# Kernel optimization log

Hardware: AMD Instinct MI355X
Metric: run time of the kernel (lower is better)

Reference implementation:

```python
import jax, jax.numpy as jnp
import numpy as np

B, S, D = 4, 2048, 1024
H, HD = 16, 64  # num_head, head_dim


def setup_inputs() -> dict:
    key = jax.random.key(0)
    k0, k1, k2, k3, k4 = jax.random.split(key, 5)
    scale = 1.0 / np.sqrt(D)
    return {
        "x": jax.random.normal(k0, (B, S, D), dtype=jnp.float32),
        "Wq": jax.random.normal(k1, (D, H * HD), dtype=jnp.float32) * scale,
        "Wk": jax.random.normal(k2, (D, H * HD), dtype=jnp.float32) * scale,
        "Wv": jax.random.normal(k3, (D, H * HD), dtype=jnp.float32) * scale,
        "Wo": jax.random.normal(k4, (H * HD, H * HD), dtype=jnp.float32) * scale,
    }


def reference(x, Wq, Wk, Wv, Wo):
    b, s, _ = x.shape
    # projections -> [b, h, s, hd]
    q = (x @ Wq).reshape(b, s, H, HD).transpose(0, 2, 1, 3)
    k = (x @ Wk).reshape(b, s, H, HD).transpose(0, 2, 1, 3)
    v = (x @ Wv).reshape(b, s, H, HD).transpose(0, 2, 1, 3)
    # scaled scores [b, h, s, s]
    scores = jnp.einsum("bhqd,bhkd->bhqk", q, k) / np.sqrt(HD).astype(np.float32)
    causal = jnp.triu(jnp.ones((s, s), dtype=bool), k=1)  # True above diagonal
    scores = jnp.where(causal, -jnp.inf, scores)
    att = jax.nn.softmax(scores, axis=-1)
    # dropout p=0.0 -> identity
    out = jnp.einsum("bhqk,bhkd->bqhd", att, v).reshape(b, s, H * HD)
    return out @ Wo
```

## Files before the change

### kernel.cpp

```cpp
#include <hip/hip_runtime.h>


typedef __attribute__((ext_vector_type(8))) short short8_t;
typedef __attribute__((ext_vector_type(4))) short short4_t;
typedef __attribute__((ext_vector_type(4))) float float4_t;

constexpr int Bz = 4, Sq = 2048, Dm = 1024, NH = 16, HD = 64;

#define GLOAD_LDS16(g, l)                                                      \
  __builtin_amdgcn_global_load_lds(                                            \
      (const __attribute__((address_space(1))) unsigned int*)(g),              \
      (__attribute__((address_space(3))) unsigned int*)(l), 16, 0, 0)

__device__ __forceinline__ unsigned short f2bf(float f) {
  unsigned u = __builtin_bit_cast(unsigned, f);
  u += 0x7fffu + ((u >> 16) & 1u);
  return (unsigned short)(u >> 16);
}

__device__ __forceinline__ float exp2_fast(float x) {
#if __has_builtin(__builtin_amdgcn_exp2f)
  return __builtin_amdgcn_exp2f(x);
#else
  return exp2f(x);
#endif
}

__device__ __forceinline__ float m3(float a, float b, float c) {
  return fmaxf(fmaxf(a, b), c);
}

__global__ __launch_bounds__(256) void cast_x_kernel(const float* __restrict__ x,
                                                     unsigned short* __restrict__ xb) {
  size_t i = (size_t)blockIdx.x * 256 + threadIdx.x;
  float4 v = ((const float4*)x)[i];
  ushort4 o;
  o.x = f2bf(v.x); o.y = f2bf(v.y); o.z = f2bf(v.z); o.w = f2bf(v.w);
  ((ushort4*)xb)[i] = o;
}

__global__ __launch_bounds__(256) void transpose_w_kernel(
    const float* __restrict__ Wq, const float* __restrict__ Wk,
    const float* __restrict__ Wv, const float* __restrict__ Wo,
    unsigned short* __restrict__ wqT, unsigned short* __restrict__ wkT,
    unsigned short* __restrict__ wvT, unsigned short* __restrict__ woT) {
  __shared__ float tile[64][65];
  int zz = blockIdx.z;
  const float* W = zz == 0 ? Wq : (zz == 1 ? Wk : (zz == 2 ? Wv : Wo));
  unsigned short* WT = zz == 0 ? wqT : (zz == 1 ? wkT : (zz == 2 ? wvT : woT));
  int n0 = blockIdx.x * 64, k0 = blockIdx.y * 64;
  int tx = threadIdx.x & 63, ty = threadIdx.x >> 6;
#pragma unroll
  for (int i = 0; i < 16; ++i) {
    int r = i * 4 + ty;
    tile[r][tx] = W[(size_t)(k0 + r) * Dm + n0 + tx];
  }
  __syncthreads();
#pragma unroll
  for (int i = 0; i < 16; ++i) {
    int r = i * 4 + ty;
    WT[(size_t)(n0 + r) * Dm + k0 + tx] = f2bf(tile[tx][r]);
  }
}

#define SBAR do { __builtin_amdgcn_sched_barrier(0); __builtin_amdgcn_s_barrier(); } while (0)
#define VMW(n_) asm volatile("s_waitcnt vmcnt(" #n_ ")" ::: "memory")

#define STGA2(buf_, kt_) do {                                                  \
  GLOAD_LDS16(gA + (size_t)lrow * Dm + (kt_) * 64 + csA,                       \
              smA + (buf_) * 8192 + tid * 8);                                  \
  GLOAD_LDS16(gA + (size_t)(lrow + 64) * Dm + (kt_) * 64 + csA,                \
              smA + (buf_) * 8192 + 4096 + tid * 8);                           \
} while (0)
#define STGB4(buf_, kt_) do {                                                  \
  GLOAD_LDS16(gB + (size_t)lrow * Dm + (kt_) * 64 + csA,                       \
              smB + (buf_) * 16384 + tid * 8);                                 \
  GLOAD_LDS16(gB + (size_t)(lrow + 64) * Dm + (kt_) * 64 + csA,                \
              smB + (buf_) * 16384 + 4096 + tid * 8);                          \
  GLOAD_LDS16(gB + (size_t)(lrow + 128) * Dm + (kt_) * 64 + csA,               \
              smB + (buf_) * 16384 + 8192 + tid * 8);                          \
  GLOAD_LDS16(gB + (size_t)(lrow + 192) * Dm + (kt_) * 64 + csA,               \
              smB + (buf_) * 16384 + 12288 + tid * 8);                         \
} while (0)
#define LDA8(buf_) do {                                                        \
  _Pragma("unroll") for (int i_ = 0; i_ < 4; ++i_) {                           \
    const unsigned short* p_ = smA + (buf_) * 8192 + aoff + i_ * 1024;         \
    a[i_][0] = *(const short8_t*)(p_ + csw0);                                  \
    a[i_][1] = *(const short8_t*)(p_ + csw1);                                  \
  }                                                                            \
} while (0)
#define LDB4(dst_, buf_, jh_) do {                                             \
  _Pragma("unroll") for (int j_ = 0; j_ < 2; ++j_) {                           \
    const unsigned short* p_ =                                                 \
        smB + (buf_) * 16384 + boff + ((jh_) * 2 + j_) * 1024;                 \
    dst_[j_][0] = *(const short8_t*)(p_ + csw0);                               \
    dst_[j_][1] = *(const short8_t*)(p_ + csw1);                               \
  }                                                                            \
} while (0)
#define MF16(breg_, joff_) do {                                                \
  __builtin_amdgcn_s_setprio(1);                                               \
  _Pragma("unroll") for (int i_ = 0; i_ < 4; ++i_)                             \
  _Pragma("unroll") for (int j_ = 0; j_ < 2; ++j_) {                           \
    acc[i_][(joff_) + j_] = __builtin_amdgcn_mfma_f32_16x16x32_bf16(           \
        a[i_][0], breg_[j_][0], acc[i_][(joff_) + j_], 0, 0, 0);               \
    acc[i_][(joff_) + j_] = __builtin_amdgcn_mfma_f32_16x16x32_bf16(           \
        a[i_][1], breg_[j_][1], acc[i_][(joff_) + j_], 0, 0, 0);               \
  }                                                                            \
  __builtin_amdgcn_s_setprio(0);                                               \
} while (0)

__device__ __forceinline__ void gemm128x256_mainloop(
    const unsigned short* __restrict__ A, const unsigned short* __restrict__ BT,
    int m0, int n0, unsigned short* smA, unsigned short* smB, float4_t acc[4][4]) {
  const int tid = threadIdx.x;
  const int lane = tid & 63, lr = lane & 15, quad = lane >> 4;
  const int wid = tid >> 6, wm = wid >> 2, wn = wid & 3;
  const int aoff = (wm * 64 + lr) * 64;
  const int boff = (wn * 64 + lr) * 64;
  const int csw0 = (quad ^ (lr & 7)) * 8;
  const int csw1 = csw0 ^ 32;
  const int lrow = tid >> 3;
  const int csA = ((tid & 7) ^ (lrow & 7)) * 8;
  const unsigned short* gA = A + (size_t)m0 * Dm;
  const unsigned short* gB = BT + (size_t)n0 * Dm;

  short8_t a[4][2], bA[2][2], bB[2][2];

  STGA2(0, 0); STGB4(0, 0); STGA2(1, 1);
  VMW(2); SBAR;

#pragma unroll 1
  for (int T = 0; T < 7; ++T) {
    const int t1 = 2 * T + 1, t2 = 2 * T + 2, t3 = 2 * T + 3;
    LDA8(0); LDB4(bA, 0, 0); STGB4(1, t1); SBAR; MF16(bA, 0); SBAR;
    LDB4(bB, 0, 1); STGA2(0, t2); SBAR; MF16(bB, 2); VMW(2); SBAR;
    LDA8(1); LDB4(bA, 1, 0); STGB4(0, t2); SBAR; MF16(bA, 0); SBAR;
    LDB4(bB, 1, 1); STGA2(1, t3); SBAR; MF16(bB, 2); VMW(2); SBAR;
  }
  LDA8(0); LDB4(bA, 0, 0); STGB4(1, 15); SBAR; MF16(bA, 0); SBAR;
  LDB4(bB, 0, 1); SBAR; MF16(bB, 2); VMW(0); SBAR;
  LDA8(1); LDB4(bA, 1, 0); SBAR; MF16(bA, 0); SBAR;
  LDB4(bB, 1, 1); SBAR; MF16(bB, 2);
}

__global__ __launch_bounds__(512, 2) void gemm_qkv_kernel(
    const unsigned short* __restrict__ xb,
    const unsigned short* __restrict__ wqT, const unsigned short* __restrict__ wkT,
    const unsigned short* __restrict__ wvT,
    unsigned short* __restrict__ qb, unsigned short* __restrict__ kb,
    unsigned short* __restrict__ vt) {
  __shared__ unsigned short smA[2 * 8192];
  __shared__ unsigned short smB[2 * 16384];
  int lin = (int)blockIdx.x;
  int logical = (lin & 7) * 96 + (lin >> 3);
  int bx = logical & 3;
  int by = (logical >> 2) & 63;
  int bz = logical >> 8;
  const unsigned short* WT = bz == 0 ? wqT : (bz == 1 ? wkT : wvT);
  unsigned short* outb = bz == 0 ? qb : (bz == 1 ? kb : vt);
  bool isV = bz == 2;
  float qscale = (bz == 0) ? 0.18033688011112042f : 1.0f;
  int m0 = by * 128, n0 = bx * 256;
  float4_t z = {0.f, 0.f, 0.f, 0.f};
  float4_t acc[4][4];
#pragma unroll
  for (int i = 0; i < 4; ++i)
#pragma unroll
    for (int j = 0; j < 4; ++j) acc[i][j] = z;
  gemm128x256_mainloop(xb, WT, m0, n0, smA, smB, acc);

  const int lane = threadIdx.x & 63, lr = lane & 15, quad = lane >> 4;
  const int wid = threadIdx.x >> 6, wm = wid >> 2, wn = wid & 3;
  const int mb = m0 + wm * 64 + quad * 4;
  const int nb = n0 + wn * 64 + lr;
  if (isV) {
#pragma unroll
    for (int ai = 0; ai < 4; ++ai)
#pragma unroll
      for (int bj = 0; bj < 4; ++bj) {
        int m = mb + ai * 16;
        int n = nb + bj * 16;
        int b = m >> 11, s = m & (Sq - 1);
        int h = n >> 6, hd = n & (HD - 1);
        ushort4 pk;
        pk.x = f2bf(acc[ai][bj][0]); pk.y = f2bf(acc[ai][bj][1]);
        pk.z = f2bf(acc[ai][bj][2]); pk.w = f2bf(acc[ai][bj][3]);
        *(ushort4*)(outb + (((size_t)b * NH + h) * HD + hd) * Sq + s) = pk;
      }
  } else {
#pragma unroll
    for (int ai = 0; ai < 4; ++ai)
#pragma unroll
      for (int bj = 0; bj < 4; ++bj)
#pragma unroll
        for (int r = 0; r < 4; ++r) {
          int m = mb + ai * 16 + r;
          int n = nb + bj * 16;
          int b = m >> 11, s = m & (Sq - 1);
          int h = n >> 6, hd = n & (HD - 1);
          outb[(((size_t)b * NH + h) * Sq + s) * HD + hd] = f2bf(acc[ai][bj][r] * qscale);
        }
  }
}

__global__ __launch_bounds__(512, 2) void gemm_out_kernel(
    const unsigned short* __restrict__ ao, const unsigned short* __restrict__ woT,
    float* __restrict__ out) {
  __shared__ unsigned short smA[2 * 8192];
  __shared__ unsigned short smB[2 * 16384];
  int lin = (int)blockIdx.x;
  int logical = (lin & 7) * 32 + (lin >> 3);
  int bx = logical & 3;
  int by = logical >> 2;
  int m0 = by * 128, n0 = bx * 256;
  float4_t z = {0.f, 0.f, 0.f, 0.f};
  float4_t acc[4][4];
#pragma unroll
  for (int i = 0; i < 4; ++i)
#pragma unroll
    for (int j = 0; j < 4; ++j) acc[i][j] = z;
  gemm128x256_mainloop(ao, woT, m0, n0, smA, smB, acc);

  const int lane = threadIdx.x & 63, lr = lane & 15, quad = lane >> 4;
  const int wid = threadIdx.x >> 6, wm = wid >> 2, wn = wid & 3;
  const int mb = m0 + wm * 64 + quad * 4;
  const int nb = n0 + wn * 64 + lr;
#pragma unroll
  for (int ai = 0; ai < 4; ++ai)
#pragma unroll
    for (int bj = 0; bj < 4; ++bj)
#pragma unroll
      for (int r = 0; r < 4; ++r) {
        int m = mb + ai * 16 + r;
        int n = nb + bj * 16;
        out[(size_t)m * Dm + n] = acc[ai][bj][r];
      }
}

__global__ __launch_bounds__(256) void attn_kernel(
    const unsigned short* __restrict__ qbuf, const unsigned short* __restrict__ kbuf,
    const unsigned short* __restrict__ vtbuf, unsigned short* __restrict__ ao) {
  __shared__ unsigned short lk[2 * 64 * 64];
  __shared__ unsigned short lv[2 * 64 * 64];
  int tid = threadIdx.x;
  int bh = blockIdx.x;
  int ti = 31 - (int)blockIdx.y;
  int wave = tid >> 6, lane = tid & 63;
  int lcol = lane & 15, quad = lane >> 4;
  int lc7 = lcol & 7;
  const unsigned short* Q = qbuf + (size_t)bh * Sq * HD;
  const unsigned short* K = kbuf + (size_t)bh * Sq * HD;
  const unsigned short* Vt = vtbuf + (size_t)bh * HD * Sq;
  int b = bh >> 4, h = bh & 15;
  float4_t z = {0.f, 0.f, 0.f, 0.f};

  const int r0 = tid >> 3;
  const int sgk = (tid & 7) ^ (r0 & 7);
  const unsigned short* kg = K + (size_t)r0 * HD + sgk * 8;
  const int kdst = tid * 8;

  const int w0 = (tid & 7) * 2;
  const int xa = r0 & 15;
  const int d0 = w0 ^ xa;
  const unsigned short* vsrc = Vt + (size_t)r0 * Sq + w0 * 4;
  const int vdst = r0 * 64 + d0 * 4;

  const int koff0 = (quad ^ lc7) * 8;
  const int koff1 = ((quad | 4) ^ lc7) * 8;
  int voff[4];
#pragma unroll
  for (int s4 = 0; s4 < 4; ++s4) voff[s4] = ((s4 * 4 + quad) ^ lcol) * 4;

  unsigned short* lkc = lk;
  unsigned short* lkn = lk + 4096;
  unsigned short* lvc = lv;
  unsigned short* lvn = lv + 4096;

  int q0w = ti * 64 + wave * 16;
  int q_global = q0w + lcol;
  short8_t qf0 = *(const short8_t*)(Q + (size_t)(q0w + lcol) * HD + quad * 8);
  short8_t qf1 = *(const short8_t*)(Q + (size_t)(q0w + lcol) * HD + 32 + quad * 8);
  float m_i = -INFINITY, l_i = 0.f;
  float4_t o[4];
#pragma unroll
  for (int f = 0; f < 4; ++f) o[f] = z;

  {
    GLOAD_LDS16(kg, lkc + kdst);
    GLOAD_LDS16(kg + (size_t)32 * HD, lkc + 2048 + kdst);
    short4_t a0 = *(const short4_t*)(vsrc);
    short4_t a1 = *(const short4_t*)(vsrc + 4);
    short4_t b0 = *(const short4_t*)(vsrc + (size_t)32 * Sq);
    short4_t b1 = *(const short4_t*)(vsrc + (size_t)32 * Sq + 4);
    *(short4_t*)(lvc + vdst) = a0;
    *(short4_t*)(lvc + (vdst ^ 4)) = a1;
    *(short4_t*)(lvc + vdst + 2048) = b0;
    *(short4_t*)(lvc + (vdst ^ 4) + 2048) = b1;
  }
  __syncthreads();

  int nkt = ti + 1;
  for (int kt = 0; kt < nkt; ++kt) {
    bool has_next = (kt + 1 < nkt);
    short4_t a0, a1, b0, b1;
    if (has_next) {
      const unsigned short* vs = vsrc + (size_t)(kt + 1) * 64;
      a0 = *(const short4_t*)(vs);
      a1 = *(const short4_t*)(vs + 4);
      b0 = *(const short4_t*)(vs + (size_t)32 * Sq);
      b1 = *(const short4_t*)(vs + (size_t)32 * Sq + 4);
      const unsigned short* kgn = kg + (size_t)(kt + 1) * 64 * HD;
      GLOAD_LDS16(kgn, lkn + kdst);
      GLOAD_LDS16(kgn + (size_t)32 * HD, lkn + 2048 + kdst);
    }

    float s[16];
#pragma unroll
    for (int s4 = 0; s4 < 4; ++s4) {
      const unsigned short* kr = lkc + (s4 * 16 + lcol) * 64;
      short8_t kf0 = *(const short8_t*)(kr + koff0);
      short8_t kf1 = *(const short8_t*)(kr + koff1);
      float4_t st = z;
      st = __builtin_amdgcn_mfma_f32_16x16x32_bf16(kf0, qf0, st, 0, 0, 0);
      st = __builtin_amdgcn_mfma_f32_16x16x32_bf16(kf1, qf1, st, 0, 0, 0);
#pragma unroll
      for (int r = 0; r < 4; ++r) s[s4 * 4 + r] = st[r];
    }
    if (kt == ti) {
      int key0 = kt * 64;
#pragma unroll
      for (int s4 = 0; s4 < 4; ++s4)
#pragma unroll
        for (int r = 0; r < 4; ++r)
          if (key0 + s4 * 16 + quad * 4 + r > q_global) s[s4 * 4 + r] = -INFINITY;
    }

    float ta = m3(s[0], s[1], s[2]);
    float tb = m3(s[3], s[4], s[5]);
    float tc = m3(s[6], s[7], s[8]);
    float td = m3(s[9], s[10], s[11]);
    float te = m3(s[12], s[13], s[14]);
    float tmax = m3(ta, tb, tc);
    tmax = m3(tmax, td, te);
    tmax = fmaxf(tmax, s[15]);
    tmax = fmaxf(tmax, __shfl_xor(tmax, 16, 64));
    tmax = fmaxf(tmax, __shfl_xor(tmax, 32, 64));

    if (__any(tmax > m_i + 8.f)) {
      float m_new = fmaxf(m_i, tmax);
      float alpha = exp2_fast(m_i - m_new);
      l_i *= alpha;
      m_i = m_new;
      float at[4];
#pragma unroll
      for (int r = 0; r < 4; ++r) at[r] = __shfl(alpha, quad * 4 + r, 64);
#pragma unroll
      for (int f = 0; f < 4; ++f)
#pragma unroll
        for (int r = 0; r < 4; ++r) o[f][r] *= at[r];
    }

    float psum = 0.f;
    short4_t pf[4];
#pragma unroll
    for (int s4 = 0; s4 < 4; ++s4) {
      float p0 = exp2_fast(s[s4 * 4 + 0] - m_i);
      float p1 = exp2_fast(s[s4 * 4 + 1] - m_i);
      float p2 = exp2_fast(s[s4 * 4 + 2] - m_i);
      float p3 = exp2_fast(s[s4 * 4 + 3] - m_i);
      psum += (p0 + p1) + (p2 + p3);
      unsigned lo, hi;
      asm("v_cvt_pk_bf16_f32 %0, %1, %2" : "=v"(lo) : "v"(p0), "v"(p1));
      asm("v_cvt_pk_bf16_f32 %0, %1, %2" : "=v"(hi) : "v"(p2), "v"(p3));
      uint2 packed;
      packed.x = lo;
      packed.y = hi;
      pf[s4] = __builtin_bit_cast(short4_t, packed);
    }
    psum += __shfl_xor(psum, 16, 64);
    psum += __shfl_xor(psum, 32, 64);
    l_i += psum;

    if (has_next) {
      *(short4_t*)(lvn + vdst) = a0;
      *(short4_t*)(lvn + (vdst ^ 4)) = a1;
      *(short4_t*)(lvn + vdst + 2048) = b0;
      *(short4_t*)(lvn + (vdst ^ 4) + 2048) = b1;
    }

#pragma unroll
    for (int f = 0; f < 4; ++f) {
      const unsigned short* vr = lvc + (f * 16 + lcol) * 64;
#pragma unroll
      for (int s4 = 0; s4 < 4; ++s4) {
        short4_t vf = *(const short4_t*)(vr + voff[s4]);
        o[f] = __builtin_amdgcn_mfma_f32_16x16x16bf16_1k(pf[s4], vf, o[f], 0, 0, 0);
      }
    }

    __syncthreads();
    unsigned short* t;
    t = lkc; lkc = lkn; lkn = t;
    t = lvc; lvc = lvn; lvn = t;
  }

  float lt[4];
#pragma unroll
  for (int r = 0; r < 4; ++r) lt[r] = 1.f / __shfl(l_i, quad * 4 + r, 64);
#pragma unroll
  for (int f = 0; f < 4; ++f)
#pragma unroll
    for (int r = 0; r < 4; ++r) {
      int q = q0w + quad * 4 + r;
      int hd = f * 16 + lcol;
      ao[((size_t)b * Sq + q) * (NH * HD) + h * HD + hd] = f2bf(o[f][r] * lt[r]);
    }
}

extern "C" void kernel_launch(void* const* d_in, const int* in_sizes, int n_in,
                              void* d_out, int out_size, void* d_ws, size_t ws_size,
                              hipStream_t stream) {
  const float* x = (const float*)d_in[0];
  const float* Wq = (const float*)d_in[1];
  const float* Wk = (const float*)d_in[2];
  const float* Wv = (const float*)d_in[3];
  const float* Wo = (const float*)d_in[4];
  float* out = (float*)d_out;

  char* ws = (char*)d_ws;
  size_t off = 0;
  auto carve = [&](size_t bytes) {
    void* p = ws + off;
    off += (bytes + 255) & ~(size_t)255;
    return p;
  };
  const size_t xe = (size_t)Bz * Sq * Dm;
  const size_t we = (size_t)Dm * Dm;
  unsigned short* xb = (unsigned short*)carve(xe * 2);
  unsigned short* wqT = (unsigned short*)carve(we * 2);
  unsigned short* wkT = (unsigned short*)carve(we * 2);
  unsigned short* wvT = (unsigned short*)carve(we * 2);
  unsigned short* woT = (unsigned short*)carve(we * 2);
  unsigned short* qb = (unsigned short*)carve(xe * 2);
  unsigned short* kb = (unsigned short*)carve(xe * 2);
  unsigned short* vt = (unsigned short*)carve(xe * 2);
  unsigned short* ao = (unsigned short*)carve(xe * 2);
  (void)ws_size;

  cast_x_kernel<<<xe / 4 / 256, 256, 0, stream>>>(x, xb);
  transpose_w_kernel<<<dim3(16, 16, 4), 256, 0, stream>>>(Wq, Wk, Wv, Wo,
                                                          wqT, wkT, wvT, woT);
  gemm_qkv_kernel<<<768, 512, 0, stream>>>(xb, wqT, wkT, wvT, qb, kb, vt);
  attn_kernel<<<dim3(Bz * NH, 32), 256, 0, stream>>>(qb, kb, vt, ao);
  gemm_out_kernel<<<256, 512, 0, stream>>>(ao, woT, out);
}
```

Measured before the change: 249.6 us.

## Process 128 queries per attention block with two query tiles per wave

Each attention block now covers 128 query rows instead of 64, with every wave holding two 16-row query fragments and two sets of softmax state. Each K/V tile loaded into shared memory is reused for twice as many queries, halving K/V global traffic and the number of blocks. Waves whose queries are all before the current key tile skip compute, but they still take part in loads and barriers. The grid halves to 1024 blocks, and the extra accumulators raise register pressure, which may lower occupancy.

Result: no change. 246.7 us (-1.2%).

```diff
diff --git a/kernel.cpp b/kernel.cpp
--- a/kernel.cpp
+++ b/kernel.cpp
@@ -244,7 +244,7 @@
   __shared__ unsigned short lv[2 * 64 * 64];
   int tid = threadIdx.x;
   int bh = blockIdx.x;
-  int ti = 31 - (int)blockIdx.y;
+  int ti = 15 - (int)blockIdx.y;
   int wave = tid >> 6, lane = tid & 63;
   int lcol = lane & 15, quad = lane >> 4;
   int lc7 = lcol & 7;
@@ -276,14 +276,20 @@
   unsigned short* lvc = lv;
   unsigned short* lvn = lv + 4096;
 
-  int q0w = ti * 64 + wave * 16;
-  int q_global = q0w + lcol;
-  short8_t qf0 = *(const short8_t*)(Q + (size_t)(q0w + lcol) * HD + quad * 8);
-  short8_t qf1 = *(const short8_t*)(Q + (size_t)(q0w + lcol) * HD + 32 + quad * 8);
-  float m_i = -INFINITY, l_i = 0.f;
-  float4_t o[4];
-#pragma unroll
-  for (int f = 0; f < 4; ++f) o[f] = z;
+  int q0w = ti * 128 + wave * 32;
+  int qg0 = q0w + lcol;
+  int qg1 = q0w + 16 + lcol;
+  const unsigned short* Qb0 = Q + (size_t)qg0 * HD;
+  const unsigned short* Qb1 = Q + (size_t)qg1 * HD;
+  short8_t qf0 = *(const short8_t*)(Qb0 + quad * 8);
+  short8_t qf1 = *(const short8_t*)(Qb0 + 32 + quad * 8);
+  short8_t qf2 = *(const short8_t*)(Qb1 + quad * 8);
+  short8_t qf3 = *(const short8_t*)(Qb1 + 32 + quad * 8);
+  float mi0 = -INFINITY, li0 = 0.f;
+  float mi1 = -INFINITY, li1 = 0.f;
+  float4_t o0[4], o1[4];
+#pragma unroll
+  for (int f = 0; f < 4; ++f) { o0[f] = z; o1[f] = z; }
 
   {
     GLOAD_LDS16(kg, lkc + kdst);
@@ -299,102 +305,153 @@
   }
   __syncthreads();
 
-  int nkt = ti + 1;
+  int nkt = 2 * ti + 2;
   for (int kt = 0; kt < nkt; ++kt) {
+    int key0 = kt * 64;
     bool has_next = (kt + 1 < nkt);
-    short4_t a0, a1, b0, b1;
+    short4_t va0, va1, vb0, vb1;
     if (has_next) {
       const unsigned short* vs = vsrc + (size_t)(kt + 1) * 64;
-      a0 = *(const short4_t*)(vs);
-      a1 = *(const short4_t*)(vs + 4);
-      b0 = *(const short4_t*)(vs + (size_t)32 * Sq);
-      b1 = *(const short4_t*)(vs + (size_t)32 * Sq + 4);
+      va0 = *(const short4_t*)(vs);
+      va1 = *(const short4_t*)(vs + 4);
+      vb0 = *(const short4_t*)(vs + (size_t)32 * Sq);
+      vb1 = *(const short4_t*)(vs + (size_t)32 * Sq + 4);
       const unsigned short* kgn = kg + (size_t)(kt + 1) * 64 * HD;
       GLOAD_LDS16(kgn, lkn + kdst);
       GLOAD_LDS16(kgn + (size_t)32 * HD, lkn + 2048 + kdst);
     }
 
-    float s[16];
-#pragma unroll
-    for (int s4 = 0; s4 < 4; ++s4) {
-      const unsigned short* kr = lkc + (s4 * 16 + lcol) * 64;
-      short8_t kf0 = *(const short8_t*)(kr + koff0);
-      short8_t kf1 = *(const short8_t*)(kr + koff1);
-      float4_t st = z;
-      st = __builtin_amdgcn_mfma_f32_16x16x32_bf16(kf0, qf0, st, 0, 0, 0);
-      st = __builtin_amdgcn_mfma_f32_16x16x32_bf16(kf1, qf1, st, 0, 0, 0);
-#pragma unroll
-      for (int r = 0; r < 4; ++r) s[s4 * 4 + r] = st[r];
+    bool active = (key0 <= q0w + 31);
+    short4_t pf0[4], pf1[4];
+    if (active) {
+      float s0[16], s1[16];
+#pragma unroll
+      for (int s4 = 0; s4 < 4; ++s4) {
+        const unsigned short* kr = lkc + (s4 * 16 + lcol) * 64;
+        short8_t kf0 = *(const short8_t*)(kr + koff0);
+        short8_t kf1 = *(const short8_t*)(kr + koff1);
+        float4_t st0 = z, st1 = z;
+        st0 = __builtin_amdgcn_mfma_f32_16x16x32_bf16(kf0, qf0, st0, 0, 0, 0);
+        st0 = __builtin_amdgcn_mfma_f32_16x16x32_bf16(kf1, qf1, st0, 0, 0, 0);
+        st1 = __builtin_amdgcn_mfma_f32_16x16x32_bf16(kf0, qf2, st1, 0, 0, 0);
+        st1 = __builtin_amdgcn_mfma_f32_16x16x32_bf16(kf1, qf3, st1, 0, 0, 0);
+#pragma unroll
+        for (int r = 0; r < 4; ++r) { s0[s4 * 4 + r] = st0[r]; s1[s4 * 4 + r] = st1[r]; }
+      }
+      if (key0 + 63 > q0w) {
+#pragma unroll
+        for (int s4 = 0; s4 < 4; ++s4)
+#pragma unroll
+          for (int r = 0; r < 4; ++r) {
+            int key = key0 + s4 * 16 + quad * 4 + r;
+            if (key > qg0) s0[s4 * 4 + r] = -INFINITY;
+            if (key > qg1) s1[s4 * 4 + r] = -INFINITY;
+          }
+      }
+
+      {
+        float ta = m3(s0[0], s0[1], s0[2]);
+        float tb = m3(s0[3], s0[4], s0[5]);
+        float tc = m3(s0[6], s0[7], s0[8]);
+        float td = m3(s0[9], s0[10], s0[11]);
+        float te = m3(s0[12], s0[13], s0[14]);
+        float tmax = m3(ta, tb, tc);
+        tmax = m3(tmax, td, te);
+        tmax = fmaxf(tmax, s0[15]);
+        tmax = fmaxf(tmax, __shfl_xor(tmax, 16, 64));
+        tmax = fmaxf(tmax, __shfl_xor(tmax, 32, 64));
+        if (__any(tmax > mi0 + 8.f)) {
+          float m_new = fmaxf(mi0, tmax);
+          float alpha = exp2_fast(mi0 - m_new);
+          li0 *= alpha;
+          mi0 = m_new;
+          float at[4];
+#pragma unroll
+          for (int r = 0; r < 4; ++r) at[r] = __shfl(alpha, quad * 4 + r, 64);
+#pragma unroll
+          for (int f = 0; f < 4; ++f)
+#pragma unroll
+            for (int r = 0; r < 4; ++r) o0[f][r] *= at[r];
+        }
+        float psum = 0.f;
+#pragma unroll
+        for (int s4 = 0; s4 < 4; ++s4) {
+          float p0 = exp2_fast(s0[s4 * 4 + 0] - mi0);
+          float p1 = exp2_fast(s0[s4 * 4 + 1] - mi0);
+          float p2 = exp2_fast(s0[s4 * 4 + 2] - mi0);
+          float p3 = exp2_fast(s0[s4 * 4 + 3] - mi0);
+          psum += (p0 + p1) + (p2 + p3);
+          unsigned lo, hi;
+          asm("v_cvt_pk_bf16_f32 %0, %1, %2" : "=v"(lo) : "v"(p0), "v"(p1));
+          asm("v_cvt_pk_bf16_f32 %0, %1, %2" : "=v"(hi) : "v"(p2), "v"(p3));
+          uint2 packed; packed.x = lo; packed.y = hi;
+          pf0[s4] = __builtin_bit_cast(short4_t, packed);
+        }
+        psum += __shfl_xor(psum, 16, 64);
+        psum += __shfl_xor(psum, 32, 64);
+        li0 += psum;
+      }
+      {
+        float ta = m3(s1[0], s1[1], s1[2]);
+        float tb = m3(s1[3], s1[4], s1[5]);
+        float tc = m3(s1[6], s1[7], s1[8]);
+        float td = m3(s1[9], s1[10], s1[11]);
+        float te = m3(s1[12], s1[13], s1[14]);
+        float tmax = m3(ta, tb, tc);
+        tmax = m3(tmax, td, te);
+        tmax = fmaxf(tmax, s1[15]);
+        tmax = fmaxf(tmax, __shfl_xor(tmax, 16, 64));
+        tmax = fmaxf(tmax, __shfl_xor(tmax, 32, 64));
+        if (__any(tmax > mi1 + 8.f)) {
+          float m_new = fmaxf(mi1, tmax);
+          float alpha = exp2_fast(mi1 - m_new);
+          li1 *= alpha;
+          mi1 = m_new;
+          float at[4];
+#pragma unroll
+          for (int r = 0; r < 4; ++r) at[r] = __shfl(alpha, quad * 4 + r, 64);
+#pragma unroll
+          for (int f = 0; f < 4; ++f)
+#pragma unroll
+            for (int r = 0; r < 4; ++r) o1[f][r] *= at[r];
+        }
+        float psum = 0.f;
+#pragma unroll
+        for (int s4 = 0; s4 < 4; ++s4) {
+          float p0 = exp2_fast(s1[s4 * 4 + 0] - mi1);
+          float p1 = exp2_fast(s1[s4 * 4 + 1] - mi1);
+          float p2 = exp2_fast(s1[s4 * 4 + 2] - mi1);
+          float p3 = exp2_fast(s1[s4 * 4 + 3] - mi1);
+          psum += (p0 + p1) + (p2 + p3);
+          unsigned lo, hi;
+          asm("v_cvt_pk_bf16_f32 %0, %1, %2" : "=v"(lo) : "v"(p0), "v"(p1));
+          asm("v_cvt_pk_bf16_f32 %0, %1, %2" : "=v"(hi) : "v"(p2), "v"(p3));
+          uint2 packed; packed.x = lo; packed.y = hi;
+          pf1[s4] = __builtin_bit_cast(short4_t, packed);
+        }
+        psum += __shfl_xor(psum, 16, 64);
+        psum += __shfl_xor(psum, 32, 64);
+        li1 += psum;
+      }
     }
-    if (kt == ti) {
-      int key0 = kt * 64;
-#pragma unroll
-      for (int s4 = 0; s4 < 4; ++s4)
-#pragma unroll
-        for (int r = 0; r < 4; ++r)
-          if (key0 + s4 * 16 + quad * 4 + r > q_global) s[s4 * 4 + r] = -INFINITY;
+
+    if (has_next) {
+      *(short4_t*)(lvn + vdst) = va0;
+      *(short4_t*)(lvn + (vdst ^ 4)) = va1;
+      *(short4_t*)(lvn + vdst + 2048) = vb0;
+      *(short4_t*)(lvn + (vdst ^ 4) + 2048) = vb1;
     }
 
-    float ta = m3(s[0], s[1], s[2]);
-    float tb = m3(s[3], s[4], s[5]);
-    float tc = m3(s[6], s[7], s[8]);
-    float td = m3(s[9], s[10], s[11]);
-    float te = m3(s[12], s[13], s[14]);
-    float tmax = m3(ta, tb, tc);
-    tmax = m3(tmax, td, te);
-    tmax = fmaxf(tmax, s[15]);
-    tmax = fmaxf(tmax, __shfl_xor(tmax, 16, 64));
-    tmax = fmaxf(tmax, __shfl_xor(tmax, 32, 64));
-
-    if (__any(tmax > m_i + 8.f)) {
-      float m_new = fmaxf(m_i, tmax);
-      float alpha = exp2_fast(m_i - m_new);
-      l_i *= alpha;
-      m_i = m_new;
-      float at[4];
-#pragma unroll
-      for (int r = 0; r < 4; ++r) at[r] = __shfl(alpha, quad * 4 + r, 64);
-#pragma unroll
-      for (int f = 0; f < 4; ++f)
-#pragma unroll
-        for (int r = 0; r < 4; ++r) o[f][r] *= at[r];
-    }
-
-    float psum = 0.f;
-    short4_t pf[4];
-#pragma unroll
-    for (int s4 = 0; s4 < 4; ++s4) {
-      float p0 = exp2_fast(s[s4 * 4 + 0] - m_i);
-      float p1 = exp2_fast(s[s4 * 4 + 1] - m_i);
-      float p2 = exp2_fast(s[s4 * 4 + 2] - m_i);
-      float p3 = exp2_fast(s[s4 * 4 + 3] - m_i);
-      psum += (p0 + p1) + (p2 + p3);
-      unsigned lo, hi;
-      asm("v_cvt_pk_bf16_f32 %0, %1, %2" : "=v"(lo) : "v"(p0), "v"(p1));
-      asm("v_cvt_pk_bf16_f32 %0, %1, %2" : "=v"(hi) : "v"(p2), "v"(p3));
-      uint2 packed;
-      packed.x = lo;
-      packed.y = hi;
-      pf[s4] = __builtin_bit_cast(short4_t, packed);
-    }
-    psum += __shfl_xor(psum, 16, 64);
-    psum += __shfl_xor(psum, 32, 64);
-    l_i += psum;
-
-    if (has_next) {
-      *(short4_t*)(lvn + vdst) = a0;
-      *(short4_t*)(lvn + (vdst ^ 4)) = a1;
-      *(short4_t*)(lvn + vdst + 2048) = b0;
-      *(short4_t*)(lvn + (vdst ^ 4) + 2048) = b1;
-    }
-
-#pragma unroll
-    for (int f = 0; f < 4; ++f) {
-      const unsigned short* vr = lvc + (f * 16 + lcol) * 64;
-#pragma unroll
-      for (int s4 = 0; s4 < 4; ++s4) {
-        short4_t vf = *(const short4_t*)(vr + voff[s4]);
-        o[f] = __builtin_amdgcn_mfma_f32_16x16x16bf16_1k(pf[s4], vf, o[f], 0, 0, 0);
+    if (active) {
+#pragma unroll
+      for (int f = 0; f < 4; ++f) {
+        const unsigned short* vr = lvc + (f * 16 + lcol) * 64;
+#pragma unroll
+        for (int s4 = 0; s4 < 4; ++s4) {
+          short4_t vf = *(const short4_t*)(vr + voff[s4]);
+          o0[f] = __builtin_amdgcn_mfma_f32_16x16x16bf16_1k(pf0[s4], vf, o0[f], 0, 0, 0);
+          o1[f] = __builtin_amdgcn_mfma_f32_16x16x16bf16_1k(pf1[s4], vf, o1[f], 0, 0, 0);
+        }
       }
     }
 
@@ -404,16 +461,21 @@
     t = lvc; lvc = lvn; lvn = t;
   }
 
-  float lt[4];
-#pragma unroll
-  for (int r = 0; r < 4; ++r) lt[r] = 1.f / __shfl(l_i, quad * 4 + r, 64);
+  float lt0[4], lt1[4];
+#pragma unroll
+  for (int r = 0; r < 4; ++r) {
+    lt0[r] = 1.f / __shfl(li0, quad * 4 + r, 64);
+    lt1[r] = 1.f / __shfl(li1, quad * 4 + r, 64);
+  }
 #pragma unroll
   for (int f = 0; f < 4; ++f)
 #pragma unroll
     for (int r = 0; r < 4; ++r) {
-      int q = q0w + quad * 4 + r;
       int hd = f * 16 + lcol;
-      ao[((size_t)b * Sq + q) * (NH * HD) + h * HD + hd] = f2bf(o[f][r] * lt[r]);
+      int q0 = q0w + quad * 4 + r;
+      int q1 = q0w + 16 + quad * 4 + r;
+      ao[((size_t)b * Sq + q0) * (NH * HD) + h * HD + hd] = f2bf(o0[f][r] * lt0[r]);
+      ao[((size_t)b * Sq + q1) * (NH * HD) + h * HD + hd] = f2bf(o1[f][r] * lt1[r]);
     }
 }
 
@@ -451,6 +513,6 @@
   transpose_w_kernel<<<dim3(16, 16, 4), 256, 0, stream>>>(Wq, Wk, Wv, Wo,
                                                           wqT, wkT, wvT, woT);
   gemm_qkv_kernel<<<768, 512, 0, stream>>>(xb, wqT, wkT, wvT, qb, kb, vt);
-  attn_kernel<<<dim3(Bz * NH, 32), 256, 0, stream>>>(qb, kb, vt, ao);
+  attn_kernel<<<dim3(Bz * NH, 16), 256, 0, stream>>>(qb, kb, vt, ao);
   gemm_out_kernel<<<256, 512, 0, stream>>>(ao, woT, out);
 }
```
